# Performance work log

Hardware: AMD Instinct MI355X
Metric: run time of the kernel (lower is better)

## Reference

```python
import jax, jax.numpy as jnp
import numpy as np

N = 100000
E = 1000000
D = 64


def setup_inputs() -> dict:
    key = jax.random.key(0)
    k1, k2, k3 = jax.random.split(key, 3)
    x = jax.random.normal(k1, (N, D), dtype=jnp.float32)
    edge_index = jax.random.randint(k2, (2, E), 0, N, dtype=jnp.int64)
    W = jax.random.normal(k3, (D, D), dtype=jnp.float32) * (1.0 / np.sqrt(D))  # nn.Linear weight [out, in]
    return {"x": x, "edge_index": edge_index, "W": W, "num_nodes": N}


def reference(x, edge_index, W, num_nodes):
    src, dst = edge_index[0], edge_index[1]
    # in-degree (counted on dst) + self loop
    deg = jnp.zeros((num_nodes,), dtype=x.dtype).at[dst].add(1.0) + 1.0
    dis = deg ** -0.5  # deg^{-1/2}, shape [N]
    # gather src features, scale by deg_inv_sqrt[src], scatter-add to dst
    msg = x[src] * dis[src][:, None]  # [E, D]
    agg = jnp.zeros_like(x).at[dst].add(msg)  # [N, D]
    # self-loop contribution, then scale by deg_inv_sqrt on the node axis
    agg = (agg + x * dis[:, None]) * dis[:, None]
    # linear (no bias): agg @ W^T with W of shape [out, in]
    return agg @ W.T
```

## Files before the change

kernel.cpp:

```cpp
#include <hip/hip_runtime.h>

#define FD  64
#define PAD 40

typedef __attribute__((ext_vector_type(8))) short bf16x8;
typedef __attribute__((ext_vector_type(4))) float f32x4;
typedef __attribute__((ext_vector_type(4))) unsigned short ushort4v;

__device__ inline short f2bf(float f) {
    union { float f; unsigned u; } v; v.f = f;
    unsigned r = (v.u + 0x7fffu + ((v.u >> 16) & 1u)) >> 16;
    return (short)r;
}
__device__ inline float bf2f(unsigned short u) {
    union { unsigned u; float f; } v; v.u = ((unsigned)u) << 16;
    return v.f;
}

__global__ void degpos_kernel(const int* __restrict__ dst, int* __restrict__ degi,
                              unsigned short* __restrict__ pos, int E) {
    int i = blockIdx.x * blockDim.x + threadIdx.x;
    int stride = gridDim.x * blockDim.x;
    int e4 = E >> 2;
    for (int k = i; k < e4; k += stride) {
        int4 d = ((const int4*)dst)[k];
        unsigned short p0 = (unsigned short)atomicAdd(&degi[d.x], 1);
        unsigned short p1 = (unsigned short)atomicAdd(&degi[d.y], 1);
        unsigned short p2 = (unsigned short)atomicAdd(&degi[d.z], 1);
        unsigned short p3 = (unsigned short)atomicAdd(&degi[d.w], 1);
        ushort4v p = {p0, p1, p2, p3};
        ((ushort4v*)pos)[k] = p;
    }
    if (i < (E & 3)) {
        int e = (e4 << 2) + i;
        pos[e] = (unsigned short)atomicAdd(&degi[dst[e]], 1);
    }
}

#define SCAN_ELEMS 2048

__global__ void scan1_kernel(const int* __restrict__ degi, int* __restrict__ offs,
                             int* __restrict__ bsums, float* dis, int N) {
    __shared__ int tsum[256];
    int base = blockIdx.x * SCAN_ELEMS + threadIdx.x * 8;
    int v[8];
    int s = 0;
    #pragma unroll
    for (int k = 0; k < 8; ++k) {
        int idx = base + k;
        v[k] = (idx < N) ? degi[idx] : 0;
        if (dis != nullptr && idx < N) dis[idx] = rsqrtf((float)v[k] + 1.0f);
        s += v[k];
    }
    tsum[threadIdx.x] = s;
    __syncthreads();
    for (int off = 1; off < 256; off <<= 1) {
        int t = (threadIdx.x >= off) ? tsum[threadIdx.x - off] : 0;
        __syncthreads();
        tsum[threadIdx.x] += t;
        __syncthreads();
    }
    int excl = (threadIdx.x == 0) ? 0 : tsum[threadIdx.x - 1];
    #pragma unroll
    for (int k = 0; k < 8; ++k) {
        int idx = base + k;
        if (idx < N) offs[idx] = excl;
        excl += v[k];
    }
    if (threadIdx.x == 255) bsums[blockIdx.x] = tsum[255];
}

__global__ void scan2_kernel(int* __restrict__ bsums, int nb) {
    __shared__ int t[256];
    int v = (threadIdx.x < nb) ? bsums[threadIdx.x] : 0;
    t[threadIdx.x] = v;
    __syncthreads();
    for (int off = 1; off < 256; off <<= 1) {
        int u = (threadIdx.x >= off) ? t[threadIdx.x - off] : 0;
        __syncthreads();
        t[threadIdx.x] += u;
        __syncthreads();
    }
    if (threadIdx.x < nb) bsums[threadIdx.x] = (threadIdx.x == 0) ? 0 : t[threadIdx.x - 1];
}

__global__ void scan3_kernel(int* __restrict__ offs, const int* __restrict__ bsums, int N) {
    int i = blockIdx.x * blockDim.x + threadIdx.x;
    if (i < N) offs[i] += bsums[i / SCAN_ELEMS];
}

#define ZBLOCKS    768
#define FILLBLOCKS 1280

template<bool PADDED>
__global__ __launch_bounds__(256) void fill_z_fused_kernel(
        const float* __restrict__ x, const int* __restrict__ degi,
        const float* __restrict__ W, unsigned short* __restrict__ z,
        const int* __restrict__ src, const int* __restrict__ dst,
        const int* __restrict__ offs, const int* __restrict__ bsums,
        const unsigned short* __restrict__ pos, int* __restrict__ bucket,
        int N, int E) {
    if (blockIdx.x < ZBLOCKS) {
        int lane = threadIdx.x & 63;
        int r16  = lane & 15;
        int kg   = lane >> 4;

        bf16x8 bfrag[4][2];
        #pragma unroll
        for (int ct = 0; ct < 4; ++ct) {
            #pragma unroll
            for (int kk = 0; kk < 2; ++kk) {
                const float* wp = W + (size_t)(ct * 16 + r16) * FD + kk * 32 + kg * 8;
                float4 w0 = *(const float4*)wp;
                float4 w1 = *(const float4*)(wp + 4);
                bf16x8 b;
                b[0] = f2bf(w0.x); b[1] = f2bf(w0.y); b[2] = f2bf(w0.z); b[3] = f2bf(w0.w);
                b[4] = f2bf(w1.x); b[5] = f2bf(w1.y); b[6] = f2bf(w1.z); b[7] = f2bf(w1.w);
                bfrag[ct][kk] = b;
            }
        }

        int wid    = blockIdx.x * 4 + (threadIdx.x >> 6);
        int nwaves = ZBLOCKS * 4;
        int tiles  = (N + 15) >> 4;

        for (int t = wid; t < tiles; t += nwaves) {
            int n0  = t << 4;
            int row = n0 + r16;
            int rl  = row < N ? row : N - 1;
            const float* xp = x + (size_t)rl * FD + kg * 8;
            float4 a00 = *(const float4*)(xp);
            float4 a01 = *(const float4*)(xp + 4);
            float4 a10 = *(const float4*)(xp + 32);
            float4 a11 = *(const float4*)(xp + 36);
            bf16x8 a0, a1;
            a0[0] = f2bf(a00.x); a0[1] = f2bf(a00.y); a0[2] = f2bf(a00.z); a0[3] = f2bf(a00.w);
            a0[4] = f2bf(a01.x); a0[5] = f2bf(a01.y); a0[6] = f2bf(a01.z); a0[7] = f2bf(a01.w);
            a1[0] = f2bf(a10.x); a1[1] = f2bf(a10.y); a1[2] = f2bf(a10.z); a1[3] = f2bf(a10.w);
            a1[4] = f2bf(a11.x); a1[5] = f2bf(a11.y); a1[6] = f2bf(a11.z); a1[7] = f2bf(a11.w);

            f32x4 acc[4];
            #pragma unroll
            for (int ct = 0; ct < 4; ++ct) {
                acc[ct] = (f32x4){0.f, 0.f, 0.f, 0.f};
                acc[ct] = __builtin_amdgcn_mfma_f32_16x16x32_bf16(a0, bfrag[ct][0], acc[ct], 0, 0, 0);
                acc[ct] = __builtin_amdgcn_mfma_f32_16x16x32_bf16(a1, bfrag[ct][1], acc[ct], 0, 0, 0);
            }

            #pragma unroll
            for (int reg = 0; reg < 4; ++reg) {
                int nr = n0 + kg * 4 + reg;
                if (nr < N) {
                    float dn = rsqrtf((float)degi[nr] + 1.0f);
                    #pragma unroll
                    for (int ct = 0; ct < 4; ++ct) {
                        z[(size_t)nr * FD + ct * 16 + r16] =
                            (unsigned short)f2bf(acc[ct][reg] * dn);
                    }
                }
            }
        }
    } else {
        int i = (blockIdx.x - ZBLOCKS) * blockDim.x + threadIdx.x;
        int stride = FILLBLOCKS * blockDim.x;
        int e4 = E >> 2;
        for (int k = i; k < e4; k += stride) {
            int4 d = ((const int4*)dst)[k];
            int4 s = ((const int4*)src)[k];
            ushort4v p = ((const ushort4v*)pos)[k];
            if (PADDED) {
                bucket[(size_t)d.x * PAD + min((int)p[0], PAD - 1)] = s.x;
                bucket[(size_t)d.y * PAD + min((int)p[1], PAD - 1)] = s.y;
                bucket[(size_t)d.z * PAD + min((int)p[2], PAD - 1)] = s.z;
                bucket[(size_t)d.w * PAD + min((int)p[3], PAD - 1)] = s.w;
            } else {
                bucket[offs[d.x] + bsums[d.x >> 11] + (int)p[0]] = s.x;
                bucket[offs[d.y] + bsums[d.y >> 11] + (int)p[1]] = s.y;
                bucket[offs[d.z] + bsums[d.z >> 11] + (int)p[2]] = s.z;
                bucket[offs[d.w] + bsums[d.w >> 11] + (int)p[3]] = s.w;
            }
        }
        if (i < (E & 3)) {
            int e = (e4 << 2) + i;
            int d = dst[e];
            if (PADDED) {
                bucket[(size_t)d * PAD + min((int)pos[e], PAD - 1)] = src[e];
            } else {
                bucket[offs[d] + bsums[d >> 11] + (int)pos[e]] = src[e];
            }
        }
    }
}

template<bool PADDED>
__global__ __launch_bounds__(256) void gather_z_kernel(
        const unsigned short* __restrict__ z, const int* __restrict__ degi,
        const int* __restrict__ bucket, const int* __restrict__ offs,
        const int* __restrict__ bsums, float* __restrict__ out, int N) {
    int wave = threadIdx.x >> 6;
    int lane = threadIdx.x & 63;
    int n = blockIdx.x * 4 + wave;
    if (n >= N) return;

    const unsigned short* zl = z + lane;
    int deg = degi[n];
    float self = bf2f(zl[(size_t)n * FD]);
    float dn   = rsqrtf((float)deg + 1.0f);

    const int* bk;
    int j, end;
    if (PADDED) {
        bk = bucket + (size_t)n * PAD;
        j = 0;
        end = min(deg, PAD);
    } else {
        bk = bucket;
        j = offs[n] + bsums[n >> 11];
        end = j + deg;
    }

    float acc = 0.0f;
    for (; j + 7 < end; j += 8) {
        int s0 = bk[j],     s1 = bk[j + 1], s2 = bk[j + 2], s3 = bk[j + 3];
        int s4 = bk[j + 4], s5 = bk[j + 5], s6 = bk[j + 6], s7 = bk[j + 7];
        float v0 = bf2f(zl[(size_t)s0 * FD]);
        float v1 = bf2f(zl[(size_t)s1 * FD]);
        float v2 = bf2f(zl[(size_t)s2 * FD]);
        float v3 = bf2f(zl[(size_t)s3 * FD]);
        float v4 = bf2f(zl[(size_t)s4 * FD]);
        float v5 = bf2f(zl[(size_t)s5 * FD]);
        float v6 = bf2f(zl[(size_t)s6 * FD]);
        float v7 = bf2f(zl[(size_t)s7 * FD]);
        acc += ((v0 + v1) + (v2 + v3)) + ((v4 + v5) + (v6 + v7));
    }
    for (; j + 3 < end; j += 4) {
        int s0 = bk[j], s1 = bk[j + 1], s2 = bk[j + 2], s3 = bk[j + 3];
        float v0 = bf2f(zl[(size_t)s0 * FD]);
        float v1 = bf2f(zl[(size_t)s1 * FD]);
        float v2 = bf2f(zl[(size_t)s2 * FD]);
        float v3 = bf2f(zl[(size_t)s3 * FD]);
        acc += (v0 + v1) + (v2 + v3);
    }
    for (; j < end; ++j) {
        acc += bf2f(zl[(size_t)bk[j] * FD]);
    }
    out[(size_t)n * FD + lane] = (acc + self) * dn;
}

__global__ void deg_kernel(const int* __restrict__ dst, int* __restrict__ degi, int E) {
    int i = blockIdx.x * blockDim.x + threadIdx.x;
    int stride = gridDim.x * blockDim.x;
    for (; i < E; i += stride) {
        atomicAdd(&degi[dst[i]], 1);
    }
}

__global__ void fill_kernel(const int* __restrict__ src, const int* __restrict__ dst,
                            const int* __restrict__ offs, int* __restrict__ cursor,
                            int* __restrict__ bucket, int E) {
    int i = blockIdx.x * blockDim.x + threadIdx.x;
    int stride = gridDim.x * blockDim.x;
    for (; i < E; i += stride) {
        int d = dst[i];
        int p = atomicAdd(&cursor[d], 1);
        bucket[offs[d] + p] = src[i];
    }
}

__global__ __launch_bounds__(256) void gather_linear_kernel(
        const float* __restrict__ x, const int* __restrict__ offs,
        const int* __restrict__ degi, const int* __restrict__ bucket,
        const float* __restrict__ dis, const float* __restrict__ W,
        float* __restrict__ out, int N) {
    __shared__ float Wt[FD][FD + 1];
    __shared__ float rows[4][FD];

    for (int t = threadIdx.x; t < FD * FD; t += 256) {
        Wt[t & 63][t >> 6] = W[t];
    }
    __syncthreads();

    int wave = threadIdx.x >> 6;
    int lane = threadIdx.x & 63;
    int n = blockIdx.x * 4 + wave;

    if (n < N) {
        int j   = offs[n];
        int end = j + degi[n];
        float acc = 0.0f;
        for (; j + 3 < end; j += 4) {
            int s0 = bucket[j], s1 = bucket[j + 1], s2 = bucket[j + 2], s3 = bucket[j + 3];
            float d0 = dis[s0], d1 = dis[s1], d2 = dis[s2], d3 = dis[s3];
            float v0 = x[(size_t)s0 * FD + lane];
            float v1 = x[(size_t)s1 * FD + lane];
            float v2 = x[(size_t)s2 * FD + lane];
            float v3 = x[(size_t)s3 * FD + lane];
            acc += v0 * d0 + v1 * d1 + v2 * d2 + v3 * d3;
        }
        for (; j < end; ++j) {
            int s = bucket[j];
            acc += x[(size_t)s * FD + lane] * dis[s];
        }
        float dn = dis[n];
        rows[wave][lane] = (acc + x[(size_t)n * FD + lane] * dn) * dn;
    }
    if (n < N) {
        float o = 0.0f;
        #pragma unroll
        for (int i = 0; i < FD; i += 4) {
            float4 r = *(const float4*)&rows[wave][i];
            o += r.x * Wt[i + 0][lane]
               + r.y * Wt[i + 1][lane]
               + r.z * Wt[i + 2][lane]
               + r.w * Wt[i + 3][lane];
        }
        out[(size_t)n * FD + lane] = o;
    }
}

extern "C" void kernel_launch(void* const* d_in, const int* in_sizes, int n_in,
                              void* d_out, int out_size, void* d_ws, size_t ws_size,
                              hipStream_t stream) {
    const float* x  = (const float*)d_in[0];
    const int*   ei = (const int*)d_in[1];
    const float* W  = (const float*)d_in[2];

    const int N = in_sizes[0] / FD;
    const int E = in_sizes[1] / 2;
    const int* src = ei;
    const int* dst = ei + E;

    float* out = (float*)d_out;
    const int nb = (N + SCAN_ELEMS - 1) / SCAN_ELEMS;

    size_t posB = (((size_t)E * 2) + 7) & ~(size_t)7;
    size_t need_pad = (size_t)N * 4 + posB + (size_t)N * PAD * 4 + (size_t)N * FD * 2;
    size_t need_csr = ((size_t)N * 2 + 1024 + (size_t)E) * 4 + posB + (size_t)N * FD * 2;

    if (ws_size >= need_pad) {
        char* ws = (char*)d_ws;
        int*   degi   = (int*)ws;    ws += (size_t)N * 4;
        unsigned short* pos = (unsigned short*)ws;  ws += posB;
        int*   bucket = (int*)ws;    ws += (size_t)N * PAD * 4;
        unsigned short* z   = (unsigned short*)ws;

        hipMemsetAsync(degi, 0, (size_t)N * 4, stream);
        degpos_kernel<<<2048, 256, 0, stream>>>(dst, degi, pos, E);
        fill_z_fused_kernel<true><<<ZBLOCKS + FILLBLOCKS, 256, 0, stream>>>(
            x, degi, W, z, src, dst, nullptr, nullptr, pos, bucket, N, E);
        gather_z_kernel<true><<<(N + 3) / 4, 256, 0, stream>>>(
            z, degi, bucket, nullptr, nullptr, out, N);
    } else if (ws_size >= need_csr) {
        char* ws = (char*)d_ws;
        int*   degi   = (int*)ws;    ws += (size_t)N * 4;
        int*   offs   = (int*)ws;    ws += (size_t)N * 4;
        int*   bsums  = (int*)ws;    ws += 1024 * 4;
        int*   bucket = (int*)ws;    ws += (size_t)E * 4;
        unsigned short* pos = (unsigned short*)ws;  ws += posB;
        unsigned short* z   = (unsigned short*)ws;

        hipMemsetAsync(degi, 0, (size_t)N * 4, stream);
        degpos_kernel<<<2048, 256, 0, stream>>>(dst, degi, pos, E);
        scan1_kernel<<<nb, 256, 0, stream>>>(degi, offs, bsums, nullptr, N);
        scan2_kernel<<<1, 256, 0, stream>>>(bsums, nb);
        fill_z_fused_kernel<false><<<ZBLOCKS + FILLBLOCKS, 256, 0, stream>>>(
            x, degi, W, z, src, dst, offs, bsums, pos, bucket, N, E);
        gather_z_kernel<false><<<(N + 3) / 4, 256, 0, stream>>>(
            z, degi, bucket, offs, bsums, out, N);
    } else {
        char* ws = (char*)d_ws;
        int*   degi   = (int*)ws;    ws += (size_t)N * 4;
        float* dis    = (float*)ws;  ws += (size_t)N * 4;
        int*   offs   = (int*)ws;    ws += (size_t)N * 4;
        int*   cursor = (int*)ws;    ws += (size_t)N * 4;
        int*   bsums  = (int*)ws;    ws += 1024 * 4;
        int*   bucket = (int*)ws;

        hipMemsetAsync(degi,   0, (size_t)N * 4, stream);
        hipMemsetAsync(cursor, 0, (size_t)N * 4, stream);
        deg_kernel<<<2048, 256, 0, stream>>>(dst, degi, E);
        scan1_kernel<<<nb, 256, 0, stream>>>(degi, offs, bsums, dis, N);
        scan2_kernel<<<1, 256, 0, stream>>>(bsums, nb);
        scan3_kernel<<<(N + 255) / 256, 256, 0, stream>>>(offs, bsums, N);
        fill_kernel<<<2048, 256, 0, stream>>>(src, dst, offs, cursor, bucket, E);
        gather_linear_kernel<<<(N + 3) / 4, 256, 0, stream>>>(
            x, offs, degi, bucket, dis, W, out, N);
    }
}
```

Before: 116.7 us.

## Overlap unscaled X·W^T GEMM with degree counting, then rescale z alongside bucket fill

The padded path now runs the MFMA projection (without degree scaling) in the same launch as the degree/position atomics, so the GEMM overlaps the atomic pass instead of waiting for it. A second fused kernel applies the deg^{-1/2} row scaling to z in place while other blocks scatter edges into buckets. This adds an extra read-modify-write pass over z and a second bf16 rounding step, which slightly changes numerics. The CSR path is split into its own kernel and its degpos grid is halved.

```diff
diff --git a/kernel.cpp b/kernel.cpp
--- a/kernel.cpp
+++ b/kernel.cpp
@@ -6,6 +6,7 @@
 typedef __attribute__((ext_vector_type(8))) short bf16x8;
 typedef __attribute__((ext_vector_type(4))) float f32x4;
 typedef __attribute__((ext_vector_type(4))) unsigned short ushort4v;
+typedef __attribute__((ext_vector_type(8))) unsigned short ushort8v;
 
 __device__ inline short f2bf(float f) {
     union { float f; unsigned u; } v; v.f = f;
@@ -17,90 +18,15 @@
     return v.f;
 }
 
-__global__ void degpos_kernel(const int* __restrict__ dst, int* __restrict__ degi,
-                              unsigned short* __restrict__ pos, int E) {
-    int i = blockIdx.x * blockDim.x + threadIdx.x;
-    int stride = gridDim.x * blockDim.x;
-    int e4 = E >> 2;
-    for (int k = i; k < e4; k += stride) {
-        int4 d = ((const int4*)dst)[k];
-        unsigned short p0 = (unsigned short)atomicAdd(&degi[d.x], 1);
-        unsigned short p1 = (unsigned short)atomicAdd(&degi[d.y], 1);
-        unsigned short p2 = (unsigned short)atomicAdd(&degi[d.z], 1);
-        unsigned short p3 = (unsigned short)atomicAdd(&degi[d.w], 1);
-        ushort4v p = {p0, p1, p2, p3};
-        ((ushort4v*)pos)[k] = p;
-    }
-    if (i < (E & 3)) {
-        int e = (e4 << 2) + i;
-        pos[e] = (unsigned short)atomicAdd(&degi[dst[e]], 1);
-    }
-}
-
-#define SCAN_ELEMS 2048
-
-__global__ void scan1_kernel(const int* __restrict__ degi, int* __restrict__ offs,
-                             int* __restrict__ bsums, float* dis, int N) {
-    __shared__ int tsum[256];
-    int base = blockIdx.x * SCAN_ELEMS + threadIdx.x * 8;
-    int v[8];
-    int s = 0;
-    #pragma unroll
-    for (int k = 0; k < 8; ++k) {
-        int idx = base + k;
-        v[k] = (idx < N) ? degi[idx] : 0;
-        if (dis != nullptr && idx < N) dis[idx] = rsqrtf((float)v[k] + 1.0f);
-        s += v[k];
-    }
-    tsum[threadIdx.x] = s;
-    __syncthreads();
-    for (int off = 1; off < 256; off <<= 1) {
-        int t = (threadIdx.x >= off) ? tsum[threadIdx.x - off] : 0;
-        __syncthreads();
-        tsum[threadIdx.x] += t;
-        __syncthreads();
-    }
-    int excl = (threadIdx.x == 0) ? 0 : tsum[threadIdx.x - 1];
-    #pragma unroll
-    for (int k = 0; k < 8; ++k) {
-        int idx = base + k;
-        if (idx < N) offs[idx] = excl;
-        excl += v[k];
-    }
-    if (threadIdx.x == 255) bsums[blockIdx.x] = tsum[255];
-}
-
-__global__ void scan2_kernel(int* __restrict__ bsums, int nb) {
-    __shared__ int t[256];
-    int v = (threadIdx.x < nb) ? bsums[threadIdx.x] : 0;
-    t[threadIdx.x] = v;
-    __syncthreads();
-    for (int off = 1; off < 256; off <<= 1) {
-        int u = (threadIdx.x >= off) ? t[threadIdx.x - off] : 0;
-        __syncthreads();
-        t[threadIdx.x] += u;
-        __syncthreads();
-    }
-    if (threadIdx.x < nb) bsums[threadIdx.x] = (threadIdx.x == 0) ? 0 : t[threadIdx.x - 1];
-}
-
-__global__ void scan3_kernel(int* __restrict__ offs, const int* __restrict__ bsums, int N) {
-    int i = blockIdx.x * blockDim.x + threadIdx.x;
-    if (i < N) offs[i] += bsums[i / SCAN_ELEMS];
-}
-
-#define ZBLOCKS    768
-#define FILLBLOCKS 1280
-
-template<bool PADDED>
-__global__ __launch_bounds__(256) void fill_z_fused_kernel(
-        const float* __restrict__ x, const int* __restrict__ degi,
-        const float* __restrict__ W, unsigned short* __restrict__ z,
-        const int* __restrict__ src, const int* __restrict__ dst,
-        const int* __restrict__ offs, const int* __restrict__ bsums,
-        const unsigned short* __restrict__ pos, int* __restrict__ bucket,
+#define F1_Z 768
+#define F1_D 1024
+
+__global__ __launch_bounds__(256) void zprime_degpos_kernel(
+        const float* __restrict__ x, const float* __restrict__ W,
+        unsigned short* __restrict__ z, const int* __restrict__ dst,
+        int* __restrict__ degi, unsigned short* __restrict__ pos,
         int N, int E) {
-    if (blockIdx.x < ZBLOCKS) {
+    if (blockIdx.x < F1_Z) {
         int lane = threadIdx.x & 63;
         int r16  = lane & 15;
         int kg   = lane >> 4;
@@ -121,7 +47,7 @@
         }
 
         int wid    = blockIdx.x * 4 + (threadIdx.x >> 6);
-        int nwaves = ZBLOCKS * 4;
+        int nwaves = F1_Z * 4;
         int tiles  = (N + 15) >> 4;
 
         for (int t = wid; t < tiles; t += nwaves) {
@@ -151,43 +77,72 @@
             for (int reg = 0; reg < 4; ++reg) {
                 int nr = n0 + kg * 4 + reg;
                 if (nr < N) {
-                    float dn = rsqrtf((float)degi[nr] + 1.0f);
                     #pragma unroll
                     for (int ct = 0; ct < 4; ++ct) {
                         z[(size_t)nr * FD + ct * 16 + r16] =
-                            (unsigned short)f2bf(acc[ct][reg] * dn);
+                            (unsigned short)f2bf(acc[ct][reg]);
                     }
                 }
             }
         }
     } else {
-        int i = (blockIdx.x - ZBLOCKS) * blockDim.x + threadIdx.x;
-        int stride = FILLBLOCKS * blockDim.x;
+        int i = (blockIdx.x - F1_Z) * blockDim.x + threadIdx.x;
+        int stride = F1_D * blockDim.x;
+        int e4 = E >> 2;
+        for (int k = i; k < e4; k += stride) {
+            int4 d = ((const int4*)dst)[k];
+            unsigned short p0 = (unsigned short)atomicAdd(&degi[d.x], 1);
+            unsigned short p1 = (unsigned short)atomicAdd(&degi[d.y], 1);
+            unsigned short p2 = (unsigned short)atomicAdd(&degi[d.z], 1);
+            unsigned short p3 = (unsigned short)atomicAdd(&degi[d.w], 1);
+            ushort4v p = {p0, p1, p2, p3};
+            ((ushort4v*)pos)[k] = p;
+        }
+        if (i < (E & 3)) {
+            int e = (e4 << 2) + i;
+            pos[e] = (unsigned short)atomicAdd(&degi[dst[e]], 1);
+        }
+    }
+}
+
+#define F2_S 1024
+#define F2_F 1280
+
+__global__ __launch_bounds__(256) void scale_fill_kernel(
+        unsigned short* __restrict__ z, const int* __restrict__ degi,
+        const int* __restrict__ src, const int* __restrict__ dst,
+        const unsigned short* __restrict__ pos, int* __restrict__ bucket,
+        int N, int E) {
+    if (blockIdx.x < F2_S) {
+        int CC = (N * FD) >> 3;
+        for (int c = blockIdx.x * blockDim.x + threadIdx.x; c < CC; c += F2_S * blockDim.x) {
+            int n = c >> 3;
+            float dn = rsqrtf((float)degi[n] + 1.0f);
+            ushort8v v = ((ushort8v*)z)[c];
+            ushort8v o;
+            #pragma unroll
+            for (int q = 0; q < 8; ++q) {
+                o[q] = (unsigned short)f2bf(bf2f(v[q]) * dn);
+            }
+            ((ushort8v*)z)[c] = o;
+        }
+    } else {
+        int i = (blockIdx.x - F2_S) * blockDim.x + threadIdx.x;
+        int stride = F2_F * blockDim.x;
         int e4 = E >> 2;
         for (int k = i; k < e4; k += stride) {
             int4 d = ((const int4*)dst)[k];
             int4 s = ((const int4*)src)[k];
             ushort4v p = ((const ushort4v*)pos)[k];
-            if (PADDED) {
-                bucket[(size_t)d.x * PAD + min((int)p[0], PAD - 1)] = s.x;
-                bucket[(size_t)d.y * PAD + min((int)p[1], PAD - 1)] = s.y;
-                bucket[(size_t)d.z * PAD + min((int)p[2], PAD - 1)] = s.z;
-                bucket[(size_t)d.w * PAD + min((int)p[3], PAD - 1)] = s.w;
-            } else {
-                bucket[offs[d.x] + bsums[d.x >> 11] + (int)p[0]] = s.x;
-                bucket[offs[d.y] + bsums[d.y >> 11] + (int)p[1]] = s.y;
-                bucket[offs[d.z] + bsums[d.z >> 11] + (int)p[2]] = s.z;
-                bucket[offs[d.w] + bsums[d.w >> 11] + (int)p[3]] = s.w;
-            }
+            bucket[(size_t)d.x * PAD + min((int)p[0], PAD - 1)] = s.x;
+            bucket[(size_t)d.y * PAD + min((int)p[1], PAD - 1)] = s.y;
+            bucket[(size_t)d.z * PAD + min((int)p[2], PAD - 1)] = s.z;
+            bucket[(size_t)d.w * PAD + min((int)p[3], PAD - 1)] = s.w;
         }
         if (i < (E & 3)) {
             int e = (e4 << 2) + i;
             int d = dst[e];
-            if (PADDED) {
-                bucket[(size_t)d * PAD + min((int)pos[e], PAD - 1)] = src[e];
-            } else {
-                bucket[offs[d] + bsums[d >> 11] + (int)pos[e]] = src[e];
-            }
+            bucket[(size_t)d * PAD + min((int)pos[e], PAD - 1)] = src[e];
         }
     }
 }
@@ -247,6 +202,169 @@
     out[(size_t)n * FD + lane] = (acc + self) * dn;
 }
 
+__global__ void degpos_kernel(const int* __restrict__ dst, int* __restrict__ degi,
+                              unsigned short* __restrict__ pos, int E) {
+    int i = blockIdx.x * blockDim.x + threadIdx.x;
+    int stride = gridDim.x * blockDim.x;
+    int e4 = E >> 2;
+    for (int k = i; k < e4; k += stride) {
+        int4 d = ((const int4*)dst)[k];
+        unsigned short p0 = (unsigned short)atomicAdd(&degi[d.x], 1);
+        unsigned short p1 = (unsigned short)atomicAdd(&degi[d.y], 1);
+        unsigned short p2 = (unsigned short)atomicAdd(&degi[d.z], 1);
+        unsigned short p3 = (unsigned short)atomicAdd(&degi[d.w], 1);
+        ushort4v p = {p0, p1, p2, p3};
+        ((ushort4v*)pos)[k] = p;
+    }
+    if (i < (E & 3)) {
+        int e = (e4 << 2) + i;
+        pos[e] = (unsigned short)atomicAdd(&degi[dst[e]], 1);
+    }
+}
+
+#define SCAN_ELEMS 2048
+
+__global__ void scan1_kernel(const int* __restrict__ degi, int* __restrict__ offs,
+                             int* __restrict__ bsums, float* dis, int N) {
+    __shared__ int tsum[256];
+    int base = blockIdx.x * SCAN_ELEMS + threadIdx.x * 8;
+    int v[8];
+    int s = 0;
+    #pragma unroll
+    for (int k = 0; k < 8; ++k) {
+        int idx = base + k;
+        v[k] = (idx < N) ? degi[idx] : 0;
+        if (dis != nullptr && idx < N) dis[idx] = rsqrtf((float)v[k] + 1.0f);
+        s += v[k];
+    }
+    tsum[threadIdx.x] = s;
+    __syncthreads();
+    for (int off = 1; off < 256; off <<= 1) {
+        int t = (threadIdx.x >= off) ? tsum[threadIdx.x - off] : 0;
+        __syncthreads();
+        tsum[threadIdx.x] += t;
+        __syncthreads();
+    }
+    int excl = (threadIdx.x == 0) ? 0 : tsum[threadIdx.x - 1];
+    #pragma unroll
+    for (int k = 0; k < 8; ++k) {
+        int idx = base + k;
+        if (idx < N) offs[idx] = excl;
+        excl += v[k];
+    }
+    if (threadIdx.x == 255) bsums[blockIdx.x] = tsum[255];
+}
+
+__global__ void scan2_kernel(int* __restrict__ bsums, int nb) {
+    __shared__ int t[256];
+    int v = (threadIdx.x < nb) ? bsums[threadIdx.x] : 0;
+    t[threadIdx.x] = v;
+    __syncthreads();
+    for (int off = 1; off < 256; off <<= 1) {
+        int u = (threadIdx.x >= off) ? t[threadIdx.x - off] : 0;
+        __syncthreads();
+        t[threadIdx.x] += u;
+        __syncthreads();
+    }
+    if (threadIdx.x < nb) bsums[threadIdx.x] = (threadIdx.x == 0) ? 0 : t[threadIdx.x - 1];
+}
+
+__global__ void scan3_kernel(int* __restrict__ offs, const int* __restrict__ bsums, int N) {
+    int i = blockIdx.x * blockDim.x + threadIdx.x;
+    if (i < N) offs[i] += bsums[i / SCAN_ELEMS];
+}
+
+#define ZBLOCKS    768
+#define FILLBLOCKS 1280
+
+__global__ __launch_bounds__(256) void fill_z_csr_kernel(
+        const float* __restrict__ x, const int* __restrict__ degi,
+        const float* __restrict__ W, unsigned short* __restrict__ z,
+        const int* __restrict__ src, const int* __restrict__ dst,
+        const int* __restrict__ offs, const int* __restrict__ bsums,
+        const unsigned short* __restrict__ pos, int* __restrict__ bucket,
+        int N, int E) {
+    if (blockIdx.x < ZBLOCKS) {
+        int lane = threadIdx.x & 63;
+        int r16  = lane & 15;
+        int kg   = lane >> 4;
+
+        bf16x8 bfrag[4][2];
+        #pragma unroll
+        for (int ct = 0; ct < 4; ++ct) {
+            #pragma unroll
+            for (int kk = 0; kk < 2; ++kk) {
+                const float* wp = W + (size_t)(ct * 16 + r16) * FD + kk * 32 + kg * 8;
+                float4 w0 = *(const float4*)wp;
+                float4 w1 = *(const float4*)(wp + 4);
+                bf16x8 b;
+                b[0] = f2bf(w0.x); b[1] = f2bf(w0.y); b[2] = f2bf(w0.z); b[3] = f2bf(w0.w);
+                b[4] = f2bf(w1.x); b[5] = f2bf(w1.y); b[6] = f2bf(w1.z); b[7] = f2bf(w1.w);
+                bfrag[ct][kk] = b;
+            }
+        }
+
+        int wid    = blockIdx.x * 4 + (threadIdx.x >> 6);
+        int nwaves = ZBLOCKS * 4;
+        int tiles  = (N + 15) >> 4;
+
+        for (int t = wid; t < tiles; t += nwaves) {
+            int n0  = t << 4;
+            int row = n0 + r16;
+            int rl  = row < N ? row : N - 1;
+            const float* xp = x + (size_t)rl * FD + kg * 8;
+            float4 a00 = *(const float4*)(xp);
+            float4 a01 = *(const float4*)(xp + 4);
+            float4 a10 = *(const float4*)(xp + 32);
+            float4 a11 = *(const float4*)(xp + 36);
+            bf16x8 a0, a1;
+            a0[0] = f2bf(a00.x); a0[1] = f2bf(a00.y); a0[2] = f2bf(a00.z); a0[3] = f2bf(a00.w);
+            a0[4] = f2bf(a01.x); a0[5] = f2bf(a01.y); a0[6] = f2bf(a01.z); a0[7] = f2bf(a01.w);
+            a1[0] = f2bf(a10.x); a1[1] = f2bf(a10.y); a1[2] = f2bf(a10.z); a1[3] = f2bf(a10.w);
+            a1[4] = f2bf(a11.x); a1[5] = f2bf(a11.y); a1[6] = f2bf(a11.z); a1[7] = f2bf(a11.w);
+
+            f32x4 acc[4];
+            #pragma unroll
+            for (int ct = 0; ct < 4; ++ct) {
+                acc[ct] = (f32x4){0.f, 0.f, 0.f, 0.f};
+                acc[ct] = __builtin_amdgcn_mfma_f32_16x16x32_bf16(a0, bfrag[ct][0], acc[ct], 0, 0, 0);
+                acc[ct] = __builtin_amdgcn_mfma_f32_16x16x32_bf16(a1, bfrag[ct][1], acc[ct], 0, 0, 0);
+            }
+
+            #pragma unroll
+            for (int reg = 0; reg < 4; ++reg) {
+                int nr = n0 + kg * 4 + reg;
+                if (nr < N) {
+                    float dn = rsqrtf((float)degi[nr] + 1.0f);
+                    #pragma unroll
+                    for (int ct = 0; ct < 4; ++ct) {
+                        z[(size_t)nr * FD + ct * 16 + r16] =
+                            (unsigned short)f2bf(acc[ct][reg] * dn);
+                    }
+                }
+            }
+        }
+    } else {
+        int i = (blockIdx.x - ZBLOCKS) * blockDim.x + threadIdx.x;
+        int stride = FILLBLOCKS * blockDim.x;
+        int e4 = E >> 2;
+        for (int k = i; k < e4; k += stride) {
+            int4 d = ((const int4*)dst)[k];
+            int4 s = ((const int4*)src)[k];
+            ushort4v p = ((const ushort4v*)pos)[k];
+            bucket[offs[d.x] + bsums[d.x >> 11] + (int)p[0]] = s.x;
+            bucket[offs[d.y] + bsums[d.y >> 11] + (int)p[1]] = s.y;
+            bucket[offs[d.z] + bsums[d.z >> 11] + (int)p[2]] = s.z;
+            bucket[offs[d.w] + bsums[d.w >> 11] + (int)p[3]] = s.w;
+        }
+        if (i < (E & 3)) {
+            int e = (e4 << 2) + i;
+            int d = dst[e];
+            bucket[offs[d] + bsums[d >> 11] + (int)pos[e]] = src[e];
+        }
+    }
+}
+
 __global__ void deg_kernel(const int* __restrict__ dst, int* __restrict__ degi, int E) {
     int i = blockIdx.x * blockDim.x + threadIdx.x;
     int stride = gridDim.x * blockDim.x;
@@ -333,7 +451,7 @@
     float* out = (float*)d_out;
     const int nb = (N + SCAN_ELEMS - 1) / SCAN_ELEMS;
 
-    size_t posB = (((size_t)E * 2) + 7) & ~(size_t)7;
+    size_t posB = (((size_t)E * 2) + 15) & ~(size_t)15;
     size_t need_pad = (size_t)N * 4 + posB + (size_t)N * PAD * 4 + (size_t)N * FD * 2;
     size_t need_csr = ((size_t)N * 2 + 1024 + (size_t)E) * 4 + posB + (size_t)N * FD * 2;
 
@@ -345,9 +463,10 @@
         unsigned short* z   = (unsigned short*)ws;
 
         hipMemsetAsync(degi, 0, (size_t)N * 4, stream);
-        degpos_kernel<<<2048, 256, 0, stream>>>(dst, degi, pos, E);
-        fill_z_fused_kernel<true><<<ZBLOCKS + FILLBLOCKS, 256, 0, stream>>>(
-            x, degi, W, z, src, dst, nullptr, nullptr, pos, bucket, N, E);
+        zprime_degpos_kernel<<<F1_Z + F1_D, 256, 0, stream>>>(
+            x, W, z, dst, degi, pos, N, E);
+        scale_fill_kernel<<<F2_S + F2_F, 256, 0, stream>>>(
+            z, degi, src, dst, pos, bucket, N, E);
         gather_z_kernel<true><<<(N + 3) / 4, 256, 0, stream>>>(
             z, degi, bucket, nullptr, nullptr, out, N);
     } else if (ws_size >= need_csr) {
@@ -360,10 +479,10 @@
         unsigned short* z   = (unsigned short*)ws;
 
         hipMemsetAsync(degi, 0, (size_t)N * 4, stream);
-        degpos_kernel<<<2048, 256, 0, stream>>>(dst, degi, pos, E);
+        degpos_kernel<<<1024, 256, 0, stream>>>(dst, degi, pos, E);
         scan1_kernel<<<nb, 256, 0, stream>>>(degi, offs, bsums, nullptr, N);
         scan2_kernel<<<1, 256, 0, stream>>>(bsums, nb);
-        fill_z_fused_kernel<false><<<ZBLOCKS + FILLBLOCKS, 256, 0, stream>>>(
+        fill_z_csr_kernel<<<ZBLOCKS + FILLBLOCKS, 256, 0, stream>>>(
             x, degi, W, z, src, dst, offs, bsums, pos, bucket, N, E);
         gather_z_kernel<false><<<(N + 3) / 4, 256, 0, stream>>>(
             z, degi, bucket, offs, bsums, out, N);
```

New measurement: 118.1 us. No clear change (+1.3%).
